# Optimization experiments

Hardware: AMD Instinct MI355X
Metric: run time of the kernel (lower is better)

## Reference

```python
import jax, jax.numpy as jnp
import numpy as np

N_MEMORY = 16
FEA_DIM = 512


def setup_inputs() -> dict:
    key = jax.random.key(0)
    ks = jax.random.split(key, 8)
    b, L, d, n = 4, 4096, FEA_DIM, N_MEMORY
    scale = 1.0 / np.sqrt(d)  # ~ torch Linear default init scale
    return {
        "query": jax.random.normal(ks[0], (b, L, d), dtype=jnp.float32),
        "W1": jax.random.uniform(ks[1], (n, d, d), jnp.float32, -scale, scale),
        "b1": jax.random.uniform(ks[2], (n, d), jnp.float32, -scale, scale),
        "W2": jax.random.uniform(ks[3], (n, d, d), jnp.float32, -scale, scale),
        "b2": jax.random.uniform(ks[4], (n, d), jnp.float32, -scale, scale),
        "Wg": jax.random.uniform(ks[5], (n, d), jnp.float32, -scale, scale),
        "bg": jax.random.uniform(ks[6], (n,), jnp.float32, -scale, scale),
        "topk": 8,
    }


def reference(query, W1, b1, W2, b2, Wg, bg, topk):
    # query: [b, L, d]; stacked per-memory-slot params: W1/W2 [n, d, d], Wg [n, d]
    n = W1.shape[0]
    # per-slot LeakyReLU negative slopes: 0.01 + 0.2/n * l
    slopes = (0.01 + 0.2 / n * jnp.arange(n, dtype=query.dtype))[:, None, None, None]
    # memory_function: Linear -> LeakyReLU(slope_l) -> Linear -> Tanh, all slots at once
    h = jnp.einsum('bld,ndh->nblh', query, W1) + b1[:, None, None, :]   # [n,b,L,d]
    h = jnp.where(h >= 0, h, h * slopes)
    x = jnp.tanh(jnp.einsum('nblh,nhd->nbld', h, W2) + b2[:, None, None, :])  # [n,b,L,d]
    # gate: Linear(d,1) -> softmax over L -> topk over L -> gather -> weighted sum
    logits = jnp.einsum('nbld,nd->nbl', x, Wg) + bg[:, None, None]      # [n,b,L]
    w = jax.nn.softmax(logits, axis=-1)
    top_w, top_idx = jax.lax.top_k(w, topk)                             # [n,b,k]
    items = jnp.take_along_axis(x, top_idx[..., None], axis=2)          # [n,b,k,d]
    combined = jnp.einsum('nbkd,nbk->nbd', items, top_w)                # [n,b,d]
    m_item = jnp.transpose(combined, (1, 0, 2))                         # [b,n,d]
    # F.normalize(dim=-1), eps=1e-12
    norm = jnp.maximum(jnp.linalg.norm(m_item, axis=-1, keepdims=True), 1e-12)
    return m_item / norm
```

## Files before the change

### kernel.cpp

```cpp
#include <hip/hip_runtime.h>
#include <hip/hip_bf16.h>
#include <cstdint>
#include <cstddef>

#define NMEM 16
#define DDIM 512
#define BATCH 4
#define LSEQ 4096
#define ROWS 16384
#define NCAND 32
#define KTOP 8
#define QPAD 20

typedef __attribute__((ext_vector_type(4))) float f32x4;
typedef __attribute__((ext_vector_type(16))) float f32x16;
typedef __attribute__((ext_vector_type(8))) int int8v;

__device__ inline float fast_tanh(float x) {
    float t = __builtin_amdgcn_fmed3f(x, -3.f, 3.f);
    float t2 = t * t;
    return t * (27.f + t2) * __builtin_amdgcn_rcpf(27.f + 9.f * t2);
}

__device__ inline int8v ldg_frag(const unsigned char* p) {
    int4 x = *(const int4*)p;
    int4 y = *(const int4*)(p + 16);
    int8v v;
    v[0] = x.x; v[1] = x.y; v[2] = x.z; v[3] = x.w;
    v[4] = y.x; v[5] = y.y; v[6] = y.z; v[7] = y.w;
    return v;
}

__global__ __launch_bounds__(256)
void prep_kernel(const float* __restrict__ query,
                 const float* __restrict__ W1, const float* __restrict__ W2,
                 unsigned char* __restrict__ Q8,
                 unsigned char* __restrict__ W1T8, unsigned char* __restrict__ W2T8) {
    int blk = blockIdx.x, t = threadIdx.x;
    if (blk < 2048) {
        size_t base = ((size_t)blk * 256 + t) * 16;
        const float4* in = (const float4*)(query + base);
        int4 o; int* op = (int*)&o;
        #pragma unroll
        for (int q = 0; q < 4; ++q) {
            float4 v = in[q];
            int lo = __builtin_amdgcn_cvt_pk_fp8_f32(v.x, v.y, 0, false);
            op[q] = __builtin_amdgcn_cvt_pk_fp8_f32(v.z, v.w, lo, true);
        }
        *(int4*)(Q8 + base) = o;
    } else {
        __shared__ float tile[64][69];
        int bid = blk - 2048;
        const float* Win = W1; unsigned char* Wout = W1T8;
        if (bid >= 1024) { bid -= 1024; Win = W2; Wout = W2T8; }
        int n = bid >> 6, t64 = bid & 63;
        int dt = (t64 >> 3) << 6, jt = (t64 & 7) << 6;
        const float* inN = Win + (size_t)n * DDIM * DDIM;
        unsigned char* outN = Wout + (size_t)n * DDIM * DDIM;
        int rr = t >> 4, cc = (t & 15) * 4;
        #pragma unroll
        for (int pass = 0; pass < 4; ++pass) {
            int row = rr + pass * 16;
            float4 v = *(const float4*)(inN + (size_t)(dt + row) * DDIM + jt + cc);
            tile[row][cc] = v.x; tile[row][cc + 1] = v.y;
            tile[row][cc + 2] = v.z; tile[row][cc + 3] = v.w;
        }
        __syncthreads();
        #pragma unroll
        for (int pass = 0; pass < 4; ++pass) {
            int jl = rr + pass * 16;
            float f0 = tile[cc][jl], f1 = tile[cc + 1][jl];
            float f2 = tile[cc + 2][jl], f3 = tile[cc + 3][jl];
            int lo = __builtin_amdgcn_cvt_pk_fp8_f32(f0, f1, 0, false);
            int dw = __builtin_amdgcn_cvt_pk_fp8_f32(f2, f3, lo, true);
            *(int*)(outN + (size_t)(jt + jl) * DDIM + dt + cc) = dw;
        }
    }
}

__global__ __launch_bounds__(256, 2)
void fused_mlp_kernel(const unsigned char* __restrict__ Q8,
                      const unsigned char* __restrict__ W1T8,
                      const unsigned char* __restrict__ W2T8,
                      const float* __restrict__ b1, const float* __restrict__ b2,
                      const float* __restrict__ Wg,
                      float* __restrict__ logits)
{
    __shared__ unsigned char hbuf[128 * 512];
    __shared__ float lsum[2][128];
    const int id = blockIdx.x;
    const int n = id & 15;
    const int m0 = (id >> 4) * 128;
    const int tid = threadIdx.x, lane = tid & 63;
    const int w = tid >> 6;
    const int rh = w >> 1, ch = w & 1;
    const int l31 = lane & 31, kh = lane >> 5;
    const unsigned char* W1n = W1T8 + (size_t)n * DDIM * DDIM;
    const unsigned char* W2n = W2T8 + (size_t)n * DDIM * DDIM;
    const float slope = 0.01f + 0.0125f * n;
    const unsigned char* Aq0 = Q8 + (size_t)(m0 + rh * 64 + l31) * DDIM + kh * 32;
    const size_t wrowoff = (size_t)(ch * 64 + l31) * DDIM + kh * 32;

    #pragma unroll 1
    for (int n0 = 0; n0 < 4; ++n0) {
        f32x16 acc[2][2] = {};
        const unsigned char* Wb = W1n + (size_t)(n0 * 128) * DDIM + wrowoff;
        #pragma unroll
        for (int kt = 0; kt < 4; ++kt) {
            int8v av[2][2];
            #pragma unroll
            for (int rt = 0; rt < 2; ++rt)
                #pragma unroll
                for (int ks = 0; ks < 2; ++ks)
                    av[rt][ks] = ldg_frag(Aq0 + (size_t)rt * 32 * DDIM + kt * 128 + ks * 64);
            #pragma unroll
            for (int ks = 0; ks < 2; ++ks)
                #pragma unroll
                for (int fc = 0; fc < 2; ++fc) {
                    int8v wfr = ldg_frag(Wb + (size_t)(fc * 32) * DDIM + kt * 128 + ks * 64);
                    #pragma unroll
                    for (int rt = 0; rt < 2; ++rt)
                        acc[rt][fc] = __builtin_amdgcn_mfma_scale_f32_32x32x64_f8f6f4(
                            wfr, av[rt][ks], acc[rt][fc], 0, 0, 0,
                            0x7F7F7F7F, 0, 0x7F7F7F7F);
                }
        }
        #pragma unroll
        for (int fc = 0; fc < 2; ++fc) {
            #pragma unroll
            for (int rt = 0; rt < 2; ++rt) {
                int r = rh * 64 + rt * 32 + l31;
                #pragma unroll
                for (int q = 0; q < 4; ++q) {
                    int jb = n0 * 128 + ch * 64 + fc * 32 + 8 * q + 4 * kh;
                    float4 bias = *(const float4*)(b1 + n * DDIM + jb);
                    float v0 = acc[rt][fc][4 * q + 0] + bias.x;
                    float v1 = acc[rt][fc][4 * q + 1] + bias.y;
                    float v2 = acc[rt][fc][4 * q + 2] + bias.z;
                    float v3 = acc[rt][fc][4 * q + 3] + bias.w;
                    v0 = v0 >= 0.f ? v0 : v0 * slope;
                    v1 = v1 >= 0.f ? v1 : v1 * slope;
                    v2 = v2 >= 0.f ? v2 : v2 * slope;
                    v3 = v3 >= 0.f ? v3 : v3 * slope;
                    int lo = __builtin_amdgcn_cvt_pk_fp8_f32(v0, v1, 0, false);
                    int dw = __builtin_amdgcn_cvt_pk_fp8_f32(v2, v3, lo, true);
                    *(int*)(hbuf + r * 512 + ((((jb >> 4) ^ (r & 7)) << 4) | (jb & 15))) = dw;
                }
            }
        }
    }

    __syncthreads();

    float rowacc[2][16] = {};
    #pragma unroll 1
    for (int n0 = 0; n0 < 4; ++n0) {
        f32x16 acc[2][2] = {};
        const unsigned char* Wb = W2n + (size_t)(n0 * 128) * DDIM + wrowoff;
        #pragma unroll
        for (int kt = 0; kt < 4; ++kt) {
            #pragma unroll
            for (int ks = 0; ks < 2; ++ks) {
                int8v av[2];
                #pragma unroll
                for (int rt = 0; rt < 2; ++rt) {
                    int hrow = rh * 64 + rt * 32 + l31, hq = hrow & 7;
                    int C0 = kt * 8 + ks * 4 + 2 * kh;
                    const int4* p0 = (const int4*)(hbuf + hrow * 512 + ((C0 ^ hq) << 4));
                    const int4* p1 = (const int4*)(hbuf + hrow * 512 + (((C0 + 1) ^ hq) << 4));
                    int4 x = *p0, y = *p1;
                    av[rt][0] = x.x; av[rt][1] = x.y; av[rt][2] = x.z; av[rt][3] = x.w;
                    av[rt][4] = y.x; av[rt][5] = y.y; av[rt][6] = y.z; av[rt][7] = y.w;
                }
                #pragma unroll
                for (int fc = 0; fc < 2; ++fc) {
                    int8v wfr = ldg_frag(Wb + (size_t)(fc * 32) * DDIM + kt * 128 + ks * 64);
                    #pragma unroll
                    for (int rt = 0; rt < 2; ++rt)
                        acc[rt][fc] = __builtin_amdgcn_mfma_scale_f32_32x32x64_f8f6f4(
                            av[rt], wfr, acc[rt][fc], 0, 0, 0,
                            0x7F7F7F7F, 0, 0x7F7F7F7F);
                }
            }
        }
        #pragma unroll
        for (int fc = 0; fc < 2; ++fc) {
            int j = n0 * 128 + ch * 64 + fc * 32 + l31;
            float bias = b2[n * DDIM + j];
            float wgv = Wg[n * DDIM + j];
            #pragma unroll
            for (int rt = 0; rt < 2; ++rt)
                #pragma unroll
                for (int reg = 0; reg < 16; ++reg)
                    rowacc[rt][reg] = fmaf(fast_tanh(acc[rt][fc][reg] + bias), wgv,
                                           rowacc[rt][reg]);
        }
    }
    #pragma unroll
    for (int sh = 1; sh < 32; sh <<= 1)
        #pragma unroll
        for (int rt = 0; rt < 2; ++rt)
            #pragma unroll
            for (int reg = 0; reg < 16; ++reg)
                rowacc[rt][reg] += __shfl_xor(rowacc[rt][reg], sh);
    if (l31 == 0) {
        #pragma unroll
        for (int rt = 0; rt < 2; ++rt)
            #pragma unroll
            for (int reg = 0; reg < 16; ++reg)
                lsum[ch][rh * 64 + rt * 32 + (reg & 3) + 8 * (reg >> 2) + 4 * kh]
                    = rowacc[rt][reg];
    }
    __syncthreads();
    if (tid < 128)
        logits[(size_t)n * ROWS + m0 + tid] = lsum[0][tid] + lsum[1][tid];
}

__global__ __launch_bounds__(256)
void topcand_kernel(const float* __restrict__ logits, int* __restrict__ cand,
                    float* __restrict__ ex_logit) {
    __shared__ float lv[LSEQ];
    __shared__ float cv[128];
    __shared__ int   ci[128];
    int p = blockIdx.x, n = p >> 2, b = p & 3;
    int t = threadIdx.x, lane = t & 63, w = t >> 6;
    const float* L = logits + (size_t)n * ROWS + (size_t)b * LSEQ;
    for (int i = t; i < LSEQ; i += 256) lv[i] = L[i];
    __syncthreads();
    float mv[16];
    int base = w * 1024;
    #pragma unroll
    for (int j = 0; j < 16; ++j) mv[j] = lv[base + j * 64 + lane];
    for (int rd = 0; rd < 32; ++rd) {
        float best = mv[0]; int bj = 0;
        #pragma unroll
        for (int j = 1; j < 16; ++j)
            if (mv[j] > best) { best = mv[j]; bj = j; }
        int bidx = base + bj * 64 + lane;
        float rv = best; int ridx = bidx;
        #pragma unroll
        for (int s = 1; s < 64; s <<= 1) {
            float ov = __shfl_xor(rv, s); int oi = __shfl_xor(ridx, s);
            if (ov > rv || (ov == rv && oi < ridx)) { rv = ov; ridx = oi; }
        }
        if (lane == 0) { cv[w * 32 + rd] = rv; ci[w * 32 + rd] = ridx; }
        if (ridx == bidx) mv[bj] = -1e30f;
    }
    __syncthreads();
    if (w == 0) {
        float v2[2]; int i2[2];
        #pragma unroll
        for (int k = 0; k < 2; ++k) { v2[k] = cv[k * 64 + lane]; i2[k] = ci[k * 64 + lane]; }
        for (int rd = 0; rd < 32; ++rd) {
            float best = v2[0]; int bi = i2[0]; int bk = 0;
            if (v2[1] > best || (v2[1] == best && i2[1] < bi)) { best = v2[1]; bi = i2[1]; bk = 1; }
            float rv = best; int ridx = bi;
            #pragma unroll
            for (int s = 1; s < 64; s <<= 1) {
                float ov = __shfl_xor(rv, s); int oi = __shfl_xor(ridx, s);
                if (ov > rv || (ov == rv && oi < ridx)) { rv = ov; ridx = oi; }
            }
            if (lane == 0) cand[p * NCAND + rd] = ridx;
            if (ridx == bi) v2[bk] = -1e30f;
        }
    } else if (w == 1) {
        if (lane < NCAND) ex_logit[p * NCAND + lane] = 0.f;
    }
}

__global__ __launch_bounds__(256)
void exact_h_kernel(const float* __restrict__ query,
                    const float* __restrict__ W1, const float* __restrict__ b1,
                    const int* __restrict__ cand, float* __restrict__ ex_h) {
    __shared__ float qs[DDIM][QPAD];
    __shared__ float hpart[4][16][64];
    int blk = blockIdx.x;
    int p = blk >> 4, r4 = blk & 15;
    int ct = r4 >> 3, jc = r4 & 7;
    int n = p >> 2, b = p & 3;
    int t = threadIdx.x, jj = t & 63, dg = t >> 6;
    int j = jc * 64 + jj;
    for (int c = 0; c < 16; ++c) {
        int li = cand[p * NCAND + ct * 16 + c];
        const float* qr = query + ((size_t)b * LSEQ + li) * DDIM;
        for (int d = t; d < DDIM; d += 256) qs[d][c] = qr[d];
    }
    __syncthreads();
    const float* W1n = W1 + (size_t)n * DDIM * DDIM;
    float acc[16] = {};
    for (int d = dg * 128; d < dg * 128 + 128; ++d) {
        float wvv = W1n[(size_t)d * DDIM + j];
        const float4* qv = (const float4*)&qs[d][0];
        #pragma unroll
        for (int c4 = 0; c4 < 4; ++c4) {
            float4 q4 = qv[c4];
            acc[c4 * 4 + 0] = fmaf(q4.x, wvv, acc[c4 * 4 + 0]);
            acc[c4 * 4 + 1] = fmaf(q4.y, wvv, acc[c4 * 4 + 1]);
            acc[c4 * 4 + 2] = fmaf(q4.z, wvv, acc[c4 * 4 + 2]);
            acc[c4 * 4 + 3] = fmaf(q4.w, wvv, acc[c4 * 4 + 3]);
        }
    }
    #pragma unroll
    for (int c = 0; c < 16; ++c) hpart[dg][c][jj] = acc[c];
    __syncthreads();
    const float slope = 0.01f + 0.0125f * n;
    float bias = b1[n * DDIM + j];
    for (int cc = dg; cc < 16; cc += 4) {
        float h = hpart[0][cc][jj] + hpart[1][cc][jj] + hpart[2][cc][jj]
                + hpart[3][cc][jj] + bias;
        h = h >= 0.f ? h : h * slope;
        ex_h[((size_t)p * NCAND + ct * 16 + cc) * DDIM + j] = h;
    }
}

__global__ __launch_bounds__(256)
void exact_x_kernel(const float* __restrict__ ex_h,
                    const float* __restrict__ W2, const float* __restrict__ b2,
                    const float* __restrict__ Wg,
                    float* __restrict__ ex_x, float* __restrict__ ex_logit) {
    __shared__ float hs[DDIM][QPAD];
    __shared__ float xpart[4][16][64];
    int blk = blockIdx.x;
    int p = blk >> 4, r4 = blk & 15;
    int ct = r4 >> 3, jc = r4 & 7;
    int n = p >> 2;
    int t = threadIdx.x, jj = t & 63, dg = t >> 6;
    int j = jc * 64 + jj;
    for (int c = 0; c < 16; ++c) {
        const float* hr = ex_h + ((size_t)p * NCAND + ct * 16 + c) * DDIM;
        for (int d = t; d < DDIM; d += 256) hs[d][c] = hr[d];
    }
    __syncthreads();
    const float* W2n = W2 + (size_t)n * DDIM * DDIM;
    float acc[16] = {};
    for (int d = dg * 128; d < dg * 128 + 128; ++d) {
        float wvv = W2n[(size_t)d * DDIM + j];
        const float4* hv = (const float4*)&hs[d][0];
        #pragma unroll
        for (int c4 = 0; c4 < 4; ++c4) {
            float4 h4 = hv[c4];
            acc[c4 * 4 + 0] = fmaf(h4.x, wvv, acc[c4 * 4 + 0]);
            acc[c4 * 4 + 1] = fmaf(h4.y, wvv, acc[c4 * 4 + 1]);
            acc[c4 * 4 + 2] = fmaf(h4.z, wvv, acc[c4 * 4 + 2]);
            acc[c4 * 4 + 3] = fmaf(h4.w, wvv, acc[c4 * 4 + 3]);
        }
    }
    #pragma unroll
    for (int c = 0; c < 16; ++c) xpart[dg][c][jj] = acc[c];
    __syncthreads();
    float bias = b2[n * DDIM + j];
    float wg = Wg[n * DDIM + j];
    for (int cc = dg; cc < 16; cc += 4) {
        float a = xpart[0][cc][jj] + xpart[1][cc][jj] + xpart[2][cc][jj]
                + xpart[3][cc][jj] + bias;
        float x = tanhf(a);
        ex_x[((size_t)p * NCAND + ct * 16 + cc) * DDIM + j] = x;
        float lp = x * wg;
        #pragma unroll
        for (int s = 1; s < 64; s <<= 1) lp += __shfl_xor(lp, s);
        if (jj == 0) atomicAdd(&ex_logit[p * NCAND + ct * 16 + cc], lp);
    }
}

__global__ __launch_bounds__(64)
void final_kernel(const float* __restrict__ ex_x, const float* __restrict__ ex_logit,
                  const int* __restrict__ cand, float* __restrict__ out)
{
    __shared__ float w8s[KTOP];
    __shared__ int   s8s[KTOP];
    int p = blockIdx.x, n = p >> 2, b = p & 3;
    int t = threadIdx.x;
    float myv = (t < NCAND) ? ex_logit[p * NCAND + t] : -1e30f;
    int myidx = (t < NCAND) ? cand[p * NCAND + t] : 0x7fffffff;
    float lmax = 0.f;
    for (int k = 0; k < KTOP; ++k) {
        float rv = myv; int ridx = myidx; int rl = t;
        #pragma unroll
        for (int s = 1; s < 64; s <<= 1) {
            float ov = __shfl_xor(rv, s); int oi = __shfl_xor(ridx, s); int ol = __shfl_xor(rl, s);
            if (ov > rv || (ov == rv && oi < ridx)) { rv = ov; ridx = oi; rl = ol; }
        }
        if (k == 0) lmax = rv;
        if (t == 0) { w8s[k] = __expf(rv - lmax); s8s[k] = rl; }
        if (t == rl) myv = -1e30f;
    }
    __syncthreads();
    float cvv[8];
    float sq = 0.f;
    int idx = 0;
    for (int d = t; d < DDIM; d += 64, ++idx) {
        float s = 0.f;
        #pragma unroll
        for (int k = 0; k < KTOP; ++k)
            s = fmaf(w8s[k], ex_x[((size_t)p * NCAND + s8s[k]) * DDIM + d], s);
        cvv[idx] = s;
        sq += s * s;
    }
    #pragma unroll
    for (int s = 1; s < 64; s <<= 1) sq += __shfl_xor(sq, s);
    float norm = fmaxf(sqrtf(sq), 1e-12f);
    idx = 0;
    for (int d = t; d < DDIM; d += 64, ++idx)
        out[((size_t)b * NMEM + n) * DDIM + d] = cvv[idx] / norm;
}

extern "C" void kernel_launch(void* const* d_in, const int* in_sizes, int n_in,
                              void* d_out, int out_size, void* d_ws, size_t ws_size,
                              hipStream_t stream)
{
    const float* query = (const float*)d_in[0];
    const float* W1    = (const float*)d_in[1];
    const float* b1    = (const float*)d_in[2];
    const float* W2    = (const float*)d_in[3];
    const float* b2    = (const float*)d_in[4];
    const float* Wg    = (const float*)d_in[5];

    char* ws = (char*)d_ws;
    const size_t MB = 1024 * 1024;
    unsigned char* Q8   = (unsigned char*)(ws);
    unsigned char* W1T8 = (unsigned char*)(ws + 8 * MB);
    unsigned char* W2T8 = (unsigned char*)(ws + 12 * MB);
    float* logits   = (float*)(ws + 16 * MB);
    int*   cand     = (int*)  (ws + 17 * MB);
    float* ex_logit = (float*)(ws + 17 * MB + 16384);
    float* ex_h     = (float*)(ws + 20 * MB);
    float* ex_x     = (float*)(ws + 28 * MB);

    prep_kernel<<<4096, 256, 0, stream>>>(query, W1, W2, Q8, W1T8, W2T8);
    fused_mlp_kernel<<<2048, 256, 0, stream>>>(Q8, W1T8, W2T8, b1, b2, Wg, logits);
    topcand_kernel<<<64, 256, 0, stream>>>(logits, cand, ex_logit);
    exact_h_kernel<<<1024, 256, 0, stream>>>(query, W1, b1, cand, ex_h);
    exact_x_kernel<<<1024, 256, 0, stream>>>(ex_h, W2, b2, Wg, ex_x, ex_logit);
    final_kernel<<<64, 64, 0, stream>>>(ex_x, ex_logit, cand, (float*)d_out);
}
```

Before: 548.1 us.

## Stage weight tiles in LDS via global_load_lds instead of per-wave global fragment loads

Both GEMM phases of the fused MLP kernel now cooperatively copy each 128x128 fp8 weight tile into a swizzled shared buffer with direct global-to-LDS loads. MFMA B fragments are then read from LDS. Previously each wave pulled its fragments straight from global memory, so waves sharing a column half fetched the same weights twice. The change adds two block barriers per k-step with no double buffering, so loads and MFMAs are serialized. It also grows LDS use by 16KB, which may affect the two-blocks-per-CU occupancy target.

```diff
diff --git a/kernel.cpp b/kernel.cpp
--- a/kernel.cpp
+++ b/kernel.cpp
@@ -16,10 +16,28 @@
 typedef __attribute__((ext_vector_type(16))) float f32x16;
 typedef __attribute__((ext_vector_type(8))) int int8v;
 
+__device__ inline void gld16(const void* gptr, void* lptr) {
+    __builtin_amdgcn_global_load_lds(
+        (const __attribute__((address_space(1))) unsigned int*)gptr,
+        (__attribute__((address_space(3))) unsigned int*)lptr,
+        16, 0, 0);
+}
+
 __device__ inline float fast_tanh(float x) {
     float t = __builtin_amdgcn_fmed3f(x, -3.f, 3.f);
     float t2 = t * t;
     return t * (27.f + t2) * __builtin_amdgcn_rcpf(27.f + 9.f * t2);
+}
+
+__device__ inline int8v load_frag(const unsigned char* Ts, int row, int g, int hs) {
+    int h = (row >> hs) & 7;
+    const int4* p0 = (const int4*)(Ts + row * 128 + (((2 * g) ^ h) << 4));
+    const int4* p1 = (const int4*)(Ts + row * 128 + (((2 * g + 1) ^ h) << 4));
+    int4 x = *p0, y = *p1;
+    int8v v;
+    v[0] = x.x; v[1] = x.y; v[2] = x.z; v[3] = x.w;
+    v[4] = y.x; v[5] = y.y; v[6] = y.z; v[7] = y.w;
+    return v;
 }
 
 __device__ inline int8v ldg_frag(const unsigned char* p) {
@@ -87,7 +105,7 @@
                       float* __restrict__ logits)
 {
     __shared__ unsigned char hbuf[128 * 512];
-    __shared__ float lsum[2][128];
+    __shared__ unsigned char Bs[128 * 128];
     const int id = blockIdx.x;
     const int n = id & 15;
     const int m0 = (id >> 4) * 128;
@@ -99,31 +117,39 @@
     const unsigned char* W2n = W2T8 + (size_t)n * DDIM * DDIM;
     const float slope = 0.01f + 0.0125f * n;
     const unsigned char* Aq0 = Q8 + (size_t)(m0 + rh * 64 + l31) * DDIM + kh * 32;
-    const size_t wrowoff = (size_t)(ch * 64 + l31) * DDIM + kh * 32;
 
     #pragma unroll 1
     for (int n0 = 0; n0 < 4; ++n0) {
         f32x16 acc[2][2] = {};
-        const unsigned char* Wb = W1n + (size_t)(n0 * 128) * DDIM + wrowoff;
-        #pragma unroll
+        const unsigned char* Bg = W1n + (size_t)(n0 * 128) * DDIM;
+        #pragma unroll 1
         for (int kt = 0; kt < 4; ++kt) {
+            #pragma unroll
+            for (int i = 0; i < 4; ++i) {
+                int c = i * 256 + tid;
+                int row = c >> 3, chk = c & 7;
+                gld16(Bg + (size_t)row * DDIM + kt * 128 + ((chk ^ (row & 7)) << 4),
+                      &Bs[c * 16]);
+            }
             int8v av[2][2];
             #pragma unroll
             for (int rt = 0; rt < 2; ++rt)
                 #pragma unroll
                 for (int ks = 0; ks < 2; ++ks)
                     av[rt][ks] = ldg_frag(Aq0 + (size_t)rt * 32 * DDIM + kt * 128 + ks * 64);
+            __syncthreads();
             #pragma unroll
             for (int ks = 0; ks < 2; ++ks)
                 #pragma unroll
                 for (int fc = 0; fc < 2; ++fc) {
-                    int8v wfr = ldg_frag(Wb + (size_t)(fc * 32) * DDIM + kt * 128 + ks * 64);
+                    int8v wfr = load_frag(Bs, ch * 64 + fc * 32 + l31, ks * 2 + kh, 0);
                     #pragma unroll
                     for (int rt = 0; rt < 2; ++rt)
                         acc[rt][fc] = __builtin_amdgcn_mfma_scale_f32_32x32x64_f8f6f4(
                             wfr, av[rt][ks], acc[rt][fc], 0, 0, 0,
                             0x7F7F7F7F, 0, 0x7F7F7F7F);
                 }
+            __syncthreads();
         }
         #pragma unroll
         for (int fc = 0; fc < 2; ++fc) {
@@ -156,9 +182,17 @@
     #pragma unroll 1
     for (int n0 = 0; n0 < 4; ++n0) {
         f32x16 acc[2][2] = {};
-        const unsigned char* Wb = W2n + (size_t)(n0 * 128) * DDIM + wrowoff;
-        #pragma unroll
+        const unsigned char* Bg = W2n + (size_t)(n0 * 128) * DDIM;
+        #pragma unroll 1
         for (int kt = 0; kt < 4; ++kt) {
+            #pragma unroll
+            for (int i = 0; i < 4; ++i) {
+                int c = i * 256 + tid;
+                int row = c >> 3, chk = c & 7;
+                gld16(Bg + (size_t)row * DDIM + kt * 128 + ((chk ^ (row & 7)) << 4),
+                      &Bs[c * 16]);
+            }
+            __syncthreads();
             #pragma unroll
             for (int ks = 0; ks < 2; ++ks) {
                 int8v av[2];
@@ -174,14 +208,15 @@
                 }
                 #pragma unroll
                 for (int fc = 0; fc < 2; ++fc) {
-                    int8v wfr = ldg_frag(Wb + (size_t)(fc * 32) * DDIM + kt * 128 + ks * 64);
+                    int8v bfr = load_frag(Bs, ch * 64 + fc * 32 + l31, ks * 2 + kh, 0);
                     #pragma unroll
                     for (int rt = 0; rt < 2; ++rt)
                         acc[rt][fc] = __builtin_amdgcn_mfma_scale_f32_32x32x64_f8f6f4(
-                            av[rt], wfr, acc[rt][fc], 0, 0, 0,
+                            av[rt], bfr, acc[rt][fc], 0, 0, 0,
                             0x7F7F7F7F, 0, 0x7F7F7F7F);
                 }
             }
+            __syncthreads();
         }
         #pragma unroll
         for (int fc = 0; fc < 2; ++fc) {
@@ -203,17 +238,19 @@
             #pragma unroll
             for (int reg = 0; reg < 16; ++reg)
                 rowacc[rt][reg] += __shfl_xor(rowacc[rt][reg], sh);
+    __syncthreads();
+    float* lsum = (float*)hbuf;
     if (l31 == 0) {
         #pragma unroll
         for (int rt = 0; rt < 2; ++rt)
             #pragma unroll
             for (int reg = 0; reg < 16; ++reg)
-                lsum[ch][rh * 64 + rt * 32 + (reg & 3) + 8 * (reg >> 2) + 4 * kh]
+                lsum[ch * 128 + rh * 64 + rt * 32 + (reg & 3) + 8 * (reg >> 2) + 4 * kh]
                     = rowacc[rt][reg];
     }
     __syncthreads();
     if (tid < 128)
-        logits[(size_t)n * ROWS + m0 + tid] = lsum[0][tid] + lsum[1][tid];
+        logits[(size_t)n * ROWS + m0 + tid] = lsum[tid] + lsum[128 + tid];
 }
 
 __global__ __launch_bounds__(256)
```

Result: faster. 501.4 us (-8.5%).
